# Kernel tuning notes

Measured on AMD Instinct MI355X. Metric: run time of the kernel, lower is better.

Reference implementation:

```python
import jax, jax.numpy as jnp
import numpy as np

DIM = 384
KEY_DIM = 32
NUM_HEADS = 8
ATTN_RATIO = 4
RESOLUTION = 48
N_TOKENS = RESOLUTION * RESOLUTION  # 2304
D_V = ATTN_RATIO * KEY_DIM          # 128
NH_KD = NUM_HEADS * KEY_DIM         # 256
DH = NUM_HEADS * D_V                # 1024
SCALE = KEY_DIM ** (-0.5)


def _make_bias_idxs(res):
    # offset (|dy|,|dx|) -> unique id via dy*res+dx (bijection onto 0..res^2-1)
    coords = np.stack(np.meshgrid(np.arange(res), np.arange(res), indexing='ij'), -1).reshape(-1, 2)
    off = np.abs(coords[:, None, :] - coords[None, :, :])  # (N,N,2)
    return (off[..., 0] * res + off[..., 1]).astype(np.int32)  # (N,N)


def setup_inputs() -> dict:
    key = jax.random.key(0)
    ks = jax.random.split(key, 12)
    f32 = jnp.float32
    x = jax.random.normal(ks[0], (N_TOKENS, DIM, 1, 1), dtype=f32)
    # 1x1 convs == linear layers: weight (out, in), bias (out,)
    q_w = jax.random.normal(ks[1], (NH_KD, DIM), dtype=f32) * 0.05
    q_b = jax.random.normal(ks[2], (NH_KD,), dtype=f32) * 0.02
    k_w = jax.random.normal(ks[3], (NH_KD, DIM), dtype=f32) * 0.05
    k_b = jax.random.normal(ks[4], (NH_KD,), dtype=f32) * 0.02
    v_w = jax.random.normal(ks[5], (DH, DIM), dtype=f32) * 0.05
    v_b = jax.random.normal(ks[6], (DH,), dtype=f32) * 0.02
    proj_w = jax.random.normal(ks[7], (DIM, DH), dtype=f32) * 0.05
    proj_b = jax.random.normal(ks[8], (DIM,), dtype=f32) * 0.02
    attention_biases = jax.random.normal(ks[9], (NUM_HEADS, 1, RESOLUTION * RESOLUTION), dtype=f32) * 0.02
    bias_idxs = jnp.asarray(_make_bias_idxs(RESOLUTION))  # (N,N) int32
    return {
        'x': x, 'q_w': q_w, 'q_b': q_b, 'k_w': k_w, 'k_b': k_b,
        'v_w': v_w, 'v_b': v_b, 'proj_w': proj_w, 'proj_b': proj_b,
        'attention_biases': attention_biases, 'bias_idxs': bias_idxs,
    }


def reference(x, q_w, q_b, k_w, k_b, v_w, v_b, proj_w, proj_b, attention_biases, bias_idxs):
    N = x.shape[0]
    xf = x.reshape(N, DIM)  # H=W=1 so 1x1 conv is a matmul
    q = (xf @ q_w.T + q_b).reshape(N, NUM_HEADS, KEY_DIM).transpose(1, 0, 2)  # (H,N,kd)
    k = (xf @ k_w.T + k_b).reshape(N, NUM_HEADS, KEY_DIM).transpose(1, 0, 2)  # (H,N,kd)
    v = (xf @ v_w.T + v_b).reshape(N, NUM_HEADS, D_V).transpose(1, 0, 2)      # (H,N,dv)
    bias = attention_biases[:, 0, :][:, bias_idxs]  # gather -> (H,N,N)
    attn = jnp.einsum('hnd,hmd->hnm', q, k) * SCALE + bias
    attn = jax.nn.softmax(attn, axis=-1)
    out = jnp.einsum('hnm,hmd->hnd', attn, v)       # (H,N,dv)
    out = out.transpose(1, 0, 2).reshape(N, DH)
    y = out @ proj_w.T + proj_b
    return y.reshape(N, DIM, 1, 1)
```

## Files before the change

kernel.cpp:

```cpp
#include <hip/hip_runtime.h>

typedef unsigned short u16;
typedef unsigned int u32;
typedef short bf16x8 __attribute__((ext_vector_type(8)));
typedef float f32x4 __attribute__((ext_vector_type(4)));

#define SCALE 0.17677669529663687f

static __device__ __forceinline__ float bf2f(u16 h) {
    u32 u = ((u32)h) << 16;
    float f;
    __builtin_memcpy(&f, &u, 4);
    return f;
}
static __device__ __forceinline__ u16 f2bf(float f) {
    u32 u;
    __builtin_memcpy(&u, &f, 4);
    u += 0x7fffu + ((u >> 16) & 1u);
    return (u16)(u >> 16);
}
static __device__ __forceinline__ float IN1(const void* p, int idx, int md) {
    return md ? ((const float*)p)[idx] : bf2f(((const u16*)p)[idx]);
}

__global__ void detect_kernel(const unsigned int* __restrict__ x, int* __restrict__ mode)
{
    int lane = threadIdx.x;
    int cnt = 0;
    for (int i = lane; i < 4096; i += 64) {
        unsigned int e = (x[i] >> 7) & 0xFFu;
        cnt += (e >= 100u && e <= 140u) ? 1 : 0;
    }
    for (int off = 32; off; off >>= 1) cnt += __shfl_down(cnt, off);
    if (lane == 0) *mode = (cnt < 2048) ? 1 : 0;
}

struct ConvArgs {
    const void* src[9];
    int ofs[10];
};
__global__ __launch_bounds__(256) void convert_all(
    ConvArgs a, u16* __restrict__ dst, const int* __restrict__ mode, int total)
{
    const int md = *mode;
    int base = (blockIdx.x * 256 + threadIdx.x) * 8;
    for (int e = 0; e < 8; e++) {
        int i = base + e;
        if (i >= total) return;
        int t = 0;
        for (int j = 1; j < 9; j++) t += (i >= a.ofs[j]) ? 1 : 0;
        int idx = i - a.ofs[t];
        dst[i] = md ? f2bf(((const float*)a.src[t])[idx])
                    : ((const u16*)a.src[t])[idx];
    }
}

__global__ __launch_bounds__(256) void qkv_kernel(
    const u16* __restrict__ x,
    const u16* __restrict__ qw, const u16* __restrict__ qb,
    const u16* __restrict__ kw, const u16* __restrict__ kb,
    const u16* __restrict__ vw, const u16* __restrict__ vb,
    u16* __restrict__ qo, u16* __restrict__ kT, u16* __restrict__ vTt)
{
    __shared__ __align__(16) short As[64 * 72];
    __shared__ __align__(16) short Bs[128 * 72];
    const int tid  = threadIdx.x;
    const int lane = tid & 63;
    const int w    = tid >> 6;
    const int l15  = lane & 15, quad = lane >> 4;
    const int mT = blockIdx.y, nT = blockIdx.x;

    const u16* wp; const u16* bp; int r0, which;
    if (nT < 2)      { wp = qw; bp = qb; r0 = nT * 128;       which = 0; }
    else if (nT < 4) { wp = kw; bp = kb; r0 = (nT - 2) * 128; which = 1; }
    else             { wp = vw; bp = vb; r0 = (nT - 4) * 128; which = 2; }

    const int wm = (w >> 1) * 32, wn = (w & 1) * 64;
    const f32x4 vz = {0.f, 0.f, 0.f, 0.f};
    f32x4 acc[2][4];
    for (int mi = 0; mi < 2; mi++)
        for (int ni = 0; ni < 4; ni++) acc[mi][ni] = vz;

    const int arow = tid >> 2, aseg = tid & 3;
    const int brow = tid >> 1, bseg = tid & 1;

    for (int kk = 0; kk < 384; kk += 64) {
        for (int c = 0; c < 2; c++)
            *(bf16x8*)&As[arow * 72 + aseg * 16 + c * 8] =
                *(const bf16x8*)&x[(mT * 64 + arow) * 384 + kk + aseg * 16 + c * 8];
        for (int c = 0; c < 4; c++)
            *(bf16x8*)&Bs[brow * 72 + bseg * 32 + c * 8] =
                *(const bf16x8*)&wp[(r0 + brow) * 384 + kk + bseg * 32 + c * 8];
        __syncthreads();
        for (int s = 0; s < 2; s++) {
            bf16x8 af[2], bfr[4];
            for (int mi = 0; mi < 2; mi++)
                af[mi] = *(const bf16x8*)&As[(wm + mi * 16 + l15) * 72 + s * 32 + quad * 8];
            for (int ni = 0; ni < 4; ni++)
                bfr[ni] = *(const bf16x8*)&Bs[(wn + ni * 16 + l15) * 72 + s * 32 + quad * 8];
            for (int mi = 0; mi < 2; mi++)
                for (int ni = 0; ni < 4; ni++)
                    acc[mi][ni] = __builtin_amdgcn_mfma_f32_16x16x32_bf16(
                        af[mi], bfr[ni], acc[mi][ni], 0, 0, 0);
        }
        __syncthreads();
    }

    for (int ni = 0; ni < 4; ni++) {
        int col = r0 + wn + ni * 16 + l15;
        float bias = bf2f(bp[col]);
        for (int mi = 0; mi < 2; mi++) {
            int rowb = mT * 64 + wm + mi * 16 + quad * 4;
            for (int rr = 0; rr < 4; rr++) {
                int tok = rowb + rr;
                u16 val = f2bf(acc[mi][ni][rr] + bias);
                if (which == 0) {
                    qo[tok * 256 + col] = val;
                } else if (which == 1) {
                    int addr = (((col >> 5) * 144 + (tok >> 4)) << 9)
                             + (((col & 31) >> 3) << 7) + ((tok & 15) << 3) + (col & 7);
                    kT[addr] = val;
                } else {
                    int addr = ((((col >> 7) * 72 + (tok >> 5)) * 8 + ((col >> 4) & 7)) << 9)
                             + (((tok >> 3) & 3) << 7) + ((col & 15) << 3) + (tok & 7);
                    vTt[addr] = val;
                }
            }
        }
    }
}

__global__ __launch_bounds__(256) void attn_v6(
    const u16* __restrict__ qbuf, const u16* __restrict__ kT,
    const u16* __restrict__ vTt,  const void* __restrict__ ab,
    u16* __restrict__ obuf, const int* __restrict__ mode)
{
    __shared__ __align__(16) float abl[2304];
    __shared__ __align__(16) u16   Pl[4][2][640];
    __shared__ __align__(16) float osh[2048];
    __shared__ __align__(16) float lsh[16];

    const int tid  = threadIdx.x;
    const int lane = tid & 63;
    const int w    = tid >> 6;
    const int l15  = lane & 15, quad = lane >> 4;
    const int head = blockIdx.y;
    const int q0   = blockIdx.x * 16;
    const int md   = *mode;

    for (int i = tid; i < 2304; i += 256) abl[i] = IN1(ab, head * 2304 + i, md);
    for (int i = tid; i < 2048; i += 256) osh[i] = 0.f;
    if (tid < 16) lsh[tid] = 0.f;
    __syncthreads();

    bf16x8 qfrag = *(const bf16x8*)&qbuf[(q0 + l15) * 256 + head * 32 + quad * 8];

    int qr[4], qc[4];
    for (int r = 0; r < 4; r++) {
        int qrow = q0 + quad * 4 + r;
        qr[r] = qrow / 48; qc[r] = qrow % 48;
    }

    const f32x4 vz = {0.f, 0.f, 0.f, 0.f};
    f32x4 o[8];
    for (int vb = 0; vb < 8; vb++) o[vb] = vz;
    float ls[4] = {0.f, 0.f, 0.f, 0.f};

    const int kstart = w * 576;
    const u16* kTb = kT  + head * 73728;
    const u16* vTb = vTt + head * 294912;
    const int t16 = kstart >> 4;
    const int vt0 = kstart >> 5;

    auto score_step = [&](int tt, bf16x8 a0, bf16x8 a1) {
        int kb = kstart + tt * 32;
        f32x4 s0 = __builtin_amdgcn_mfma_f32_16x16x32_bf16(qfrag, a0, vz, 0, 0, 0);
        f32x4 s1 = __builtin_amdgcn_mfma_f32_16x16x32_bf16(qfrag, a1, vz, 0, 0, 0);
        int k0 = kb + l15, k1 = k0 + 16;
        int kr0 = k0 / 48, kc0 = k0 % 48;
        int kr1 = k1 / 48, kc1 = k1 % 48;
        u16* P = &Pl[w][tt & 1][0];
        for (int r = 0; r < 4; r++) {
            float a0f = s0[r] * SCALE + abl[abs(qr[r] - kr0) * 48 + abs(qc[r] - kc0)];
            a0f = fminf(fmaxf(a0f, -60.f), 60.f);
            float p0 = __expf(a0f);
            ls[r] += p0;
            P[(quad * 4 + r) * 40 + l15] = f2bf(p0);
            float a1f = s1[r] * SCALE + abl[abs(qr[r] - kr1) * 48 + abs(qc[r] - kc1)];
            a1f = fminf(fmaxf(a1f, -60.f), 60.f);
            float p1 = __expf(a1f);
            ls[r] += p1;
            P[(quad * 4 + r) * 40 + 16 + l15] = f2bf(p1);
        }
    };

    {
        bf16x8 c0 = *(const bf16x8*)&kTb[((t16 + 0) * 64 + lane) * 8];
        bf16x8 c1 = *(const bf16x8*)&kTb[((t16 + 1) * 64 + lane) * 8];
        score_step(0, c0, c1);
    }
    bf16x8 kA0 = *(const bf16x8*)&kTb[((t16 + 2) * 64 + lane) * 8];
    bf16x8 kA1 = *(const bf16x8*)&kTb[((t16 + 3) * 64 + lane) * 8];

    for (int t = 0; t < 18; t++) {
        bf16x8 pf = *(const bf16x8*)&Pl[w][t & 1][l15 * 40 + quad * 8];

        bf16x8 vf[8];
        for (int vb = 0; vb < 8; vb++)
            vf[vb] = *(const bf16x8*)&vTb[(((vt0 + t) * 8 + vb) * 64 + lane) * 8];

        if (t < 17) {
            int nt = (t + 2 <= 17) ? (t + 2) : 17;
            bf16x8 kB0 = *(const bf16x8*)&kTb[((t16 + nt * 2) * 64 + lane) * 8];
            bf16x8 kB1 = *(const bf16x8*)&kTb[((t16 + nt * 2 + 1) * 64 + lane) * 8];
            score_step(t + 1, kA0, kA1);
            kA0 = kB0; kA1 = kB1;
        }

        for (int vb = 0; vb < 8; vb++)
            o[vb] = __builtin_amdgcn_mfma_f32_16x16x32_bf16(pf, vf[vb], o[vb], 0, 0, 0);
    }

    for (int r = 0; r < 4; r++)
        for (int off = 1; off < 16; off <<= 1)
            ls[r] += __shfl_xor(ls[r], off);

    for (int ph = 0; ph < 4; ph++) {
        if (w == ph) {
            for (int vb = 0; vb < 8; vb++)
                for (int r = 0; r < 4; r++)
                    osh[(quad * 4 + r) * 128 + vb * 16 + l15] += o[vb][r];
            if (l15 == 0)
                for (int r = 0; r < 4; r++) lsh[quad * 4 + r] += ls[r];
        }
        __syncthreads();
    }

    for (int i = tid; i < 2048; i += 256) {
        int row = i >> 7, dv = i & 127;
        obuf[(q0 + row) * 1024 + head * 128 + dv] = f2bf(osh[i] / lsh[row]);
    }
}

__global__ __launch_bounds__(256) void proj_kernel(
    const u16* __restrict__ ob, const u16* __restrict__ pw,
    const u16* __restrict__ pb, void* __restrict__ y, const int* __restrict__ mode)
{
    __shared__ __align__(16) short As[64 * 136];
    __shared__ __align__(16) short Bs[64 * 136];
    const int tid  = threadIdx.x;
    const int lane = tid & 63;
    const int w    = tid >> 6;
    const int l15  = lane & 15, quad = lane >> 4;
    const int mT = blockIdx.y, nT = blockIdx.x;
    const int wm = (w >> 1) * 32, wn = (w & 1) * 32;
    const int md = *mode;

    const f32x4 vz = {0.f, 0.f, 0.f, 0.f};
    f32x4 acc[2][2];
    for (int mi = 0; mi < 2; mi++)
        for (int ni = 0; ni < 2; ni++) acc[mi][ni] = vz;

    const int row = tid >> 2, seg = tid & 3;
    for (int kk = 0; kk < 1024; kk += 128) {
        for (int c = 0; c < 4; c++) {
            *(bf16x8*)&As[row * 136 + seg * 32 + c * 8] =
                *(const bf16x8*)&ob[(mT * 64 + row) * 1024 + kk + seg * 32 + c * 8];
            *(bf16x8*)&Bs[row * 136 + seg * 32 + c * 8] =
                *(const bf16x8*)&pw[(nT * 64 + row) * 1024 + kk + seg * 32 + c * 8];
        }
        __syncthreads();
        for (int s = 0; s < 4; s++) {
            bf16x8 af[2], bfr[2];
            for (int mi = 0; mi < 2; mi++)
                af[mi] = *(const bf16x8*)&As[(wm + mi * 16 + l15) * 136 + s * 32 + quad * 8];
            for (int ni = 0; ni < 2; ni++)
                bfr[ni] = *(const bf16x8*)&Bs[(wn + ni * 16 + l15) * 136 + s * 32 + quad * 8];
            for (int mi = 0; mi < 2; mi++)
                for (int ni = 0; ni < 2; ni++)
                    acc[mi][ni] = __builtin_amdgcn_mfma_f32_16x16x32_bf16(
                        af[mi], bfr[ni], acc[mi][ni], 0, 0, 0);
        }
        __syncthreads();
    }

    for (int ni = 0; ni < 2; ni++) {
        int col = nT * 64 + wn + ni * 16 + l15;
        float bias = bf2f(pb[col]);
        for (int mi = 0; mi < 2; mi++) {
            int rowb = mT * 64 + wm + mi * 16 + quad * 4;
            for (int rr = 0; rr < 4; rr++) {
                float val = acc[mi][ni][rr] + bias;
                int idx = (rowb + rr) * 384 + col;
                if (md) ((float*)y)[idx] = val;
                else    ((u16*)y)[idx]   = f2bf(val);
            }
        }
    }
}

extern "C" void kernel_launch(void* const* d_in, const int* in_sizes, int n_in,
                              void* d_out, int out_size, void* d_ws, size_t ws_size,
                              hipStream_t stream)
{
    const void *x = 0, *qw = 0, *qb = 0, *kw = 0, *kb = 0;
    const void *vw = 0, *vb = 0, *pw = 0, *pb = 0, *ab = 0;
    void* scratch = 0;

    for (int i = 0; i < n_in; i++) {
        const void* p = d_in[i];
        switch (in_sizes[i]) {
            case 884736:  x  = p; break;
            case 98304:   if (!qw) qw = p; else kw = p; break;
            case 256:     if (!qb) qb = p; else kb = p; break;
            case 393216:  if (!vw) vw = p; else pw = p; break;
            case 1024:    vb = p; break;
            case 384:     pb = p; break;
            case 18432:   ab = p; break;
            case 5308416: scratch = (void*)p; break;
        }
    }
    if (!scratch) scratch = d_ws;

    u16* arena = (u16*)scratch;
    u16* cx  = arena;
    u16* cqw = arena + 884736;
    u16* cqb = arena + 983040;
    u16* ckw = arena + 983296;
    u16* ckb = arena + 1081600;
    u16* cvw = arena + 1081856;
    u16* cvb = arena + 1475072;
    u16* cpw = arena + 1476096;
    u16* cpb = arena + 1869312;
    u16* q_bf = arena + 1869696;
    u16* kT   = arena + 2459520;
    u16* vTt  = arena + 3049344;
    u16* ob   = arena + 7767936;
    int* mode = ((int*)scratch) + 5308400;

    detect_kernel<<<1, 64, 0, stream>>>((const unsigned int*)x, mode);

    ConvArgs ca;
    ca.src[0] = x;  ca.src[1] = qw; ca.src[2] = qb; ca.src[3] = kw; ca.src[4] = kb;
    ca.src[5] = vw; ca.src[6] = vb; ca.src[7] = pw; ca.src[8] = pb;
    ca.ofs[0] = 0;       ca.ofs[1] = 884736;  ca.ofs[2] = 983040;
    ca.ofs[3] = 983296;  ca.ofs[4] = 1081600; ca.ofs[5] = 1081856;
    ca.ofs[6] = 1475072; ca.ofs[7] = 1476096; ca.ofs[8] = 1869312;
    ca.ofs[9] = 1869696;
    convert_all<<<(1869696 / 8 + 255) / 256, 256, 0, stream>>>(ca, arena, mode, 1869696);

    qkv_kernel<<<dim3(12, 36), 256, 0, stream>>>(cx, cqw, cqb, ckw, ckb, cvw, cvb,
                                                 q_bf, kT, vTt);
    attn_v6<<<dim3(144, 8), 256, 0, stream>>>(q_bf, kT, vTt, ab, ob, mode);
    proj_kernel<<<dim3(6, 36), 256, 0, stream>>>(ob, cpw, cpb, d_out, mode);
}
```

Before: 170.5 us.

## Fuse fp32-to-bf16 conversion into GEMM loads and stage QKV stores through LDS

Removes the separate convert_all pass and instead converts fp32 inputs and weights to bf16 inside the qkv and proj kernels' global-to-LDS loads, avoiding an extra launch and a round trip through the workspace. The QKV epilogue now writes results into a shared-memory tile first and then emits 16-byte vector stores in the q, kT and vTt layouts, replacing scattered 2-byte global writes. The cost is more LDS per block and repeated conversion of the weights by every block that loads them.

New measurement: 187.5 us. +10.0%, slower.

```diff
diff --git a/kernel.cpp b/kernel.cpp
--- a/kernel.cpp
+++ b/kernel.cpp
@@ -22,6 +22,13 @@
 static __device__ __forceinline__ float IN1(const void* p, int idx, int md) {
     return md ? ((const float*)p)[idx] : bf2f(((const u16*)p)[idx]);
 }
+static __device__ __forceinline__ bf16x8 LD8(const void* p, int idx, int md) {
+    if (!md) return *(const bf16x8*)((const u16*)p + idx);
+    const float* f = (const float*)p + idx;
+    bf16x8 r;
+    for (int j = 0; j < 8; j++) r[j] = (short)f2bf(f[j]);
+    return r;
+}
 
 __global__ void detect_kernel(const unsigned int* __restrict__ x, int* __restrict__ mode)
 {
@@ -35,42 +42,25 @@
     if (lane == 0) *mode = (cnt < 2048) ? 1 : 0;
 }
 
-struct ConvArgs {
-    const void* src[9];
-    int ofs[10];
-};
-__global__ __launch_bounds__(256) void convert_all(
-    ConvArgs a, u16* __restrict__ dst, const int* __restrict__ mode, int total)
-{
-    const int md = *mode;
-    int base = (blockIdx.x * 256 + threadIdx.x) * 8;
-    for (int e = 0; e < 8; e++) {
-        int i = base + e;
-        if (i >= total) return;
-        int t = 0;
-        for (int j = 1; j < 9; j++) t += (i >= a.ofs[j]) ? 1 : 0;
-        int idx = i - a.ofs[t];
-        dst[i] = md ? f2bf(((const float*)a.src[t])[idx])
-                    : ((const u16*)a.src[t])[idx];
-    }
-}
-
 __global__ __launch_bounds__(256) void qkv_kernel(
-    const u16* __restrict__ x,
-    const u16* __restrict__ qw, const u16* __restrict__ qb,
-    const u16* __restrict__ kw, const u16* __restrict__ kb,
-    const u16* __restrict__ vw, const u16* __restrict__ vb,
-    u16* __restrict__ qo, u16* __restrict__ kT, u16* __restrict__ vTt)
+    const void* __restrict__ x,
+    const void* __restrict__ qw, const void* __restrict__ qb,
+    const void* __restrict__ kw, const void* __restrict__ kb,
+    const void* __restrict__ vw, const void* __restrict__ vb,
+    u16* __restrict__ qo, u16* __restrict__ kT, u16* __restrict__ vTt,
+    const int* __restrict__ mode)
 {
     __shared__ __align__(16) short As[64 * 72];
     __shared__ __align__(16) short Bs[128 * 72];
+    __shared__ __align__(16) short outS[128 * 72];
     const int tid  = threadIdx.x;
     const int lane = tid & 63;
     const int w    = tid >> 6;
     const int l15  = lane & 15, quad = lane >> 4;
     const int mT = blockIdx.y, nT = blockIdx.x;
-
-    const u16* wp; const u16* bp; int r0, which;
+    const int md = *mode;
+
+    const void* wp; const void* bp; int r0, which;
     if (nT < 2)      { wp = qw; bp = qb; r0 = nT * 128;       which = 0; }
     else if (nT < 4) { wp = kw; bp = kb; r0 = (nT - 2) * 128; which = 1; }
     else             { wp = vw; bp = vb; r0 = (nT - 4) * 128; which = 2; }
@@ -87,10 +77,10 @@
     for (int kk = 0; kk < 384; kk += 64) {
         for (int c = 0; c < 2; c++)
             *(bf16x8*)&As[arow * 72 + aseg * 16 + c * 8] =
-                *(const bf16x8*)&x[(mT * 64 + arow) * 384 + kk + aseg * 16 + c * 8];
+                LD8(x, (mT * 64 + arow) * 384 + kk + aseg * 16 + c * 8, md);
         for (int c = 0; c < 4; c++)
             *(bf16x8*)&Bs[brow * 72 + bseg * 32 + c * 8] =
-                *(const bf16x8*)&wp[(r0 + brow) * 384 + kk + bseg * 32 + c * 8];
+                LD8(wp, (r0 + brow) * 384 + kk + bseg * 32 + c * 8, md);
         __syncthreads();
         for (int s = 0; s < 2; s++) {
             bf16x8 af[2], bfr[4];
@@ -107,25 +97,45 @@
     }
 
     for (int ni = 0; ni < 4; ni++) {
-        int col = r0 + wn + ni * 16 + l15;
-        float bias = bf2f(bp[col]);
+        int colL = wn + ni * 16 + l15;
+        float bias = IN1(bp, r0 + colL, md);
         for (int mi = 0; mi < 2; mi++) {
-            int rowb = mT * 64 + wm + mi * 16 + quad * 4;
+            int tokb = wm + mi * 16 + quad * 4;
             for (int rr = 0; rr < 4; rr++) {
-                int tok = rowb + rr;
                 u16 val = f2bf(acc[mi][ni][rr] + bias);
-                if (which == 0) {
-                    qo[tok * 256 + col] = val;
-                } else if (which == 1) {
-                    int addr = (((col >> 5) * 144 + (tok >> 4)) << 9)
-                             + (((col & 31) >> 3) << 7) + ((tok & 15) << 3) + (col & 7);
-                    kT[addr] = val;
-                } else {
-                    int addr = ((((col >> 7) * 72 + (tok >> 5)) * 8 + ((col >> 4) & 7)) << 9)
-                             + (((tok >> 3) & 3) << 7) + ((col & 15) << 3) + (tok & 7);
-                    vTt[addr] = val;
-                }
+                if (which == 2) outS[colL * 72 + tokb + rr] = val;
+                else            outS[(tokb + rr) * 136 + colL] = val;
             }
+        }
+    }
+    __syncthreads();
+
+    if (which == 0) {
+        for (int i = 0; i < 4; i++) {
+            int c = tid + i * 256;
+            int tok = c >> 4, seg = c & 15;
+            *(bf16x8*)&qo[(mT * 64 + tok) * 256 + r0 + seg * 8] =
+                *(const bf16x8*)&outS[tok * 136 + seg * 8];
+        }
+    } else if (which == 1) {
+        int h0 = r0 >> 5;
+        for (int i = 0; i < 4; i++) {
+            int c = tid + i * 256;
+            int tile = c >> 6, ln = c & 63;
+            int head_loc = tile >> 2, t16_loc = tile & 3;
+            int q2 = ln >> 4, l2 = ln & 15;
+            *(bf16x8*)&kT[(((h0 + head_loc) * 144 + mT * 4 + t16_loc) << 9) + ln * 8] =
+                *(const bf16x8*)&outS[(t16_loc * 16 + l2) * 136 + head_loc * 32 + q2 * 8];
+        }
+    } else {
+        int hv = r0 >> 7;
+        for (int i = 0; i < 4; i++) {
+            int c = tid + i * 256;
+            int tile = c >> 6, ln = c & 63;
+            int kt_loc = tile >> 3, vb2 = tile & 7;
+            int q2 = ln >> 4, l2 = ln & 15;
+            *(bf16x8*)&vTt[(((hv * 72 + mT * 2 + kt_loc) * 8 + vb2) << 9) + ln * 8] =
+                *(const bf16x8*)&outS[(vb2 * 16 + l2) * 72 + kt_loc * 32 + q2 * 8];
         }
     }
 }
@@ -243,8 +253,8 @@
 }
 
 __global__ __launch_bounds__(256) void proj_kernel(
-    const u16* __restrict__ ob, const u16* __restrict__ pw,
-    const u16* __restrict__ pb, void* __restrict__ y, const int* __restrict__ mode)
+    const u16* __restrict__ ob, const void* __restrict__ pw,
+    const void* __restrict__ pb, void* __restrict__ y, const int* __restrict__ mode)
 {
     __shared__ __align__(16) short As[64 * 136];
     __shared__ __align__(16) short Bs[64 * 136];
@@ -267,7 +277,7 @@
             *(bf16x8*)&As[row * 136 + seg * 32 + c * 8] =
                 *(const bf16x8*)&ob[(mT * 64 + row) * 1024 + kk + seg * 32 + c * 8];
             *(bf16x8*)&Bs[row * 136 + seg * 32 + c * 8] =
-                *(const bf16x8*)&pw[(nT * 64 + row) * 1024 + kk + seg * 32 + c * 8];
+                LD8(pw, (nT * 64 + row) * 1024 + kk + seg * 32 + c * 8, md);
         }
         __syncthreads();
         for (int s = 0; s < 4; s++) {
@@ -286,7 +296,7 @@
 
     for (int ni = 0; ni < 2; ni++) {
         int col = nT * 64 + wn + ni * 16 + l15;
-        float bias = bf2f(pb[col]);
+        float bias = IN1(pb, col, md);
         for (int mi = 0; mi < 2; mi++) {
             int rowb = mT * 64 + wm + mi * 16 + quad * 4;
             for (int rr = 0; rr < 4; rr++) {
@@ -323,34 +333,15 @@
     if (!scratch) scratch = d_ws;
 
     u16* arena = (u16*)scratch;
-    u16* cx  = arena;
-    u16* cqw = arena + 884736;
-    u16* cqb = arena + 983040;
-    u16* ckw = arena + 983296;
-    u16* ckb = arena + 1081600;
-    u16* cvw = arena + 1081856;
-    u16* cvb = arena + 1475072;
-    u16* cpw = arena + 1476096;
-    u16* cpb = arena + 1869312;
-    u16* q_bf = arena + 1869696;
-    u16* kT   = arena + 2459520;
-    u16* vTt  = arena + 3049344;
-    u16* ob   = arena + 7767936;
+    u16* q_bf = arena;
+    u16* kT   = arena + 589824;
+    u16* vTt  = arena + 1179648;
+    u16* ob   = arena + 3538944;
     int* mode = ((int*)scratch) + 5308400;
 
     detect_kernel<<<1, 64, 0, stream>>>((const unsigned int*)x, mode);
-
-    ConvArgs ca;
-    ca.src[0] = x;  ca.src[1] = qw; ca.src[2] = qb; ca.src[3] = kw; ca.src[4] = kb;
-    ca.src[5] = vw; ca.src[6] = vb; ca.src[7] = pw; ca.src[8] = pb;
-    ca.ofs[0] = 0;       ca.ofs[1] = 884736;  ca.ofs[2] = 983040;
-    ca.ofs[3] = 983296;  ca.ofs[4] = 1081600; ca.ofs[5] = 1081856;
-    ca.ofs[6] = 1475072; ca.ofs[7] = 1476096; ca.ofs[8] = 1869312;
-    ca.ofs[9] = 1869696;
-    convert_all<<<(1869696 / 8 + 255) / 256, 256, 0, stream>>>(ca, arena, mode, 1869696);
-
-    qkv_kernel<<<dim3(12, 36), 256, 0, stream>>>(cx, cqw, cqb, ckw, ckb, cvw, cvb,
-                                                 q_bf, kT, vTt);
+    qkv_kernel<<<dim3(12, 36), 256, 0, stream>>>(x, qw, qb, kw, kb, vw, vb,
+                                                 q_bf, kT, vTt, mode);
     attn_v6<<<dim3(144, 8), 256, 0, stream>>>(q_bf, kT, vTt, ab, ob, mode);
-    proj_kernel<<<dim3(6, 36), 256, 0, stream>>>(ob, cpw, cpb, d_out, mode);
-}
+    proj_kernel<<<dim3(6, 36), 256, 0, stream>>>(ob, pw, pb, d_out, mode);
+}
```
